# Optimization experiments

Hardware: AMD Instinct MI355X
Metric: run time of the kernel (lower is better)

## Reference

```python
import jax, jax.numpy as jnp
import numpy as np

R_BLOCKS = 8  # r: number of diagonal blocks

def _rotate(Wp, R):
    # Wp: [out, in], R: [r, b, b] with in = r*b.
    # Equivalent to Wp @ block_diag(R[0],...,R[r-1]) without materializing [in,in].
    o = Wp.shape[0]
    r, b, _ = R.shape
    Wb = Wp.reshape(o, r, b)
    return jnp.einsum('ori,rij->orj', Wb, R).reshape(o, r * b)

def setup_inputs() -> dict:
    key = jax.random.key(0)
    ks = jax.random.split(key, 6)
    in_f, out_f, r = 1024, 1024, R_BLOCKS
    blk = in_f // r
    return {
        'attn': jax.random.normal(ks[0], (3 * out_f, in_f), jnp.float32) * 0.02,
        'bias': jax.random.normal(ks[1], (3 * out_f,), jnp.float32) * 0.02,
        'x': jax.random.normal(ks[2], (4, 2048, in_f), jnp.float32),
        'q_R': jax.random.normal(ks[3], (r, blk, blk), jnp.float32) * 0.02,
        'k_R': jax.random.normal(ks[4], (r, blk, blk), jnp.float32) * 0.02,
        'v_R': jax.random.normal(ks[5], (r, blk, blk), jnp.float32) * 0.02,
    }

def reference(attn, bias, x, q_R, k_R, v_R):
    # attn.data in torch detaches the frozen pretrained weight
    W = jax.lax.stop_gradient(attn)
    Wq, Wk, Wv = jnp.split(W, 3, axis=0)
    filt = jnp.concatenate([_rotate(Wq, q_R), _rotate(Wk, k_R), _rotate(Wv, v_R)], axis=0)
    # F.linear: x @ filt.T + bias -> [B, S, 3*out]
    return jnp.einsum('bsi,oi->bso', x, filt) + bias
```

## Files before the change

kernel.cpp:

```cpp
#include <hip/hip_runtime.h>
#include <hip/hip_bf16.h>
#include <stdint.h>

typedef __attribute__((ext_vector_type(8))) short short8;
typedef __attribute__((ext_vector_type(4))) float floatx4;
typedef __attribute__((ext_vector_type(16))) float floatx16;

#define M_TOT 8192
#define N_TOT 3072
#define K_TOT 1024
#define BM 128
#define BN 128
#define BK 64

__device__ inline unsigned short f2bf(float f) {
    union { float f; unsigned int ui; } v; v.f = f;
    unsigned int x = v.ui;
    unsigned int r = (x + 0x7fffu + ((x >> 16) & 1u)) >> 16;
    return (unsigned short)r;
}

__device__ inline void gl2lds16(const void* g, void* l) {
    __builtin_amdgcn_global_load_lds(
        (__attribute__((address_space(1))) void*)g,
        (__attribute__((address_space(3))) void*)l,
        16, 0, 0);
}

__global__ __launch_bounds__(256) void cvt_f32_bf16_kernel(
    const float* __restrict__ in, unsigned short* __restrict__ out, int n8)
{
    int i = blockIdx.x * 256 + threadIdx.x;
    if (i >= n8) return;
    const float4* p = (const float4*)in + (size_t)i * 2;
    float4 a = p[0], b = p[1];
    short8 s;
    s[0] = (short)f2bf(a.x); s[1] = (short)f2bf(a.y);
    s[2] = (short)f2bf(a.z); s[3] = (short)f2bf(a.w);
    s[4] = (short)f2bf(b.x); s[5] = (short)f2bf(b.y);
    s[6] = (short)f2bf(b.z); s[7] = (short)f2bf(b.w);
    *(short8*)(out + (size_t)i * 8) = s;
}

__global__ __launch_bounds__(256) void rotate_w_kernel(
    const float* __restrict__ W,
    const float* __restrict__ qR,
    const float* __restrict__ kR,
    const float* __restrict__ vR,
    unsigned short* __restrict__ Fout)
{
    __shared__ float Rs[128 * 128];
    __shared__ float Ws[64 * 132];

    const int tid = threadIdx.x;
    const int o0 = blockIdx.x * 64;
    const int r = blockIdx.y;

    const float* R = (o0 < 1024) ? qR : (o0 < 2048) ? kR : vR;
    R += (size_t)r * 128 * 128;

#pragma unroll
    for (int i = 0; i < 16; ++i) {
        int idx = (i * 256 + tid) * 4;
        *(float4*)(Rs + idx) = *(const float4*)(R + idx);
    }
#pragma unroll
    for (int i = 0; i < 8; ++i) {
        int idx = (i * 256 + tid) * 4;
        int row = idx >> 7;
        int col = idx & 127;
        *(float4*)(Ws + row * 132 + col) =
            *(const float4*)(W + (size_t)(o0 + row) * K_TOT + r * 128 + col);
    }
    __syncthreads();

    const int jg = (tid & 15) * 8;
    const int ob = tid >> 4;

    float acc[4][8];
#pragma unroll
    for (int a = 0; a < 4; ++a)
#pragma unroll
        for (int b = 0; b < 8; ++b) acc[a][b] = 0.f;

    for (int i = 0; i < 128; ++i) {
        float4 r0 = *(const float4*)(Rs + i * 128 + jg);
        float4 r1 = *(const float4*)(Rs + i * 128 + jg + 4);
        float rv[8] = {r0.x, r0.y, r0.z, r0.w, r1.x, r1.y, r1.z, r1.w};
#pragma unroll
        for (int oo = 0; oo < 4; ++oo) {
            float wv = Ws[(ob + oo * 16) * 132 + i];
#pragma unroll
            for (int t = 0; t < 8; ++t) acc[oo][t] += wv * rv[t];
        }
    }

#pragma unroll
    for (int oo = 0; oo < 4; ++oo) {
        int o = o0 + ob + oo * 16;
        short8 s;
#pragma unroll
        for (int t = 0; t < 8; ++t) s[t] = (short)f2bf(acc[oo][t]);
        *(short8*)(Fout + (size_t)o * K_TOT + r * 128 + jg) = s;
    }
}

__global__ void gemm_bt_kernel(
    const unsigned short* __restrict__ X,
    const unsigned short* __restrict__ F,
    const float* __restrict__ bias,
    float* __restrict__ out)
{
    __shared__ __align__(16) unsigned char smem[2 * BM * BK * sizeof(unsigned short)];
    unsigned short* As = (unsigned short*)smem;
    unsigned short* Bs = As + BM * BK;
    float* Cs = (float*)smem;

    const int tid = threadIdx.x;
    const int wave = tid >> 6;
    const int lane = tid & 63;
    const int m0 = blockIdx.x * BM;
    const int n0 = blockIdx.y * BN;

    const int wm = wave >> 1;
    const int wn = wave & 1;
    const int l31 = lane & 31;
    const int khalf = lane >> 5;

    const int srow_lane = lane >> 3;

    floatx16 acc[2][2];
#pragma unroll
    for (int a = 0; a < 2; ++a)
#pragma unroll
        for (int b = 0; b < 2; ++b)
#pragma unroll
            for (int t = 0; t < 16; ++t) acc[a][b][t] = 0.f;

    const int fr_read = (l31 & 7) ^ (((l31 >> 3) & 3) << 1);

    for (int k0 = 0; k0 < K_TOT; k0 += BK) {
#pragma unroll
        for (int p = 0; p < 4; ++p) {
            const int rr = (wave * 4 + p) * 8 + srow_lane;
            const int scg = (lane & 7) ^ srow_lane ^ ((((wave * 4 + p) & 3)) << 1);
            const int scol = scg * 8;
            gl2lds16(X + (size_t)(m0 + rr) * K_TOT + k0 + scol,
                     As + (wave * 4 + p) * 512 + lane * 8);
            gl2lds16(F + (size_t)(n0 + rr) * K_TOT + k0 + scol,
                     Bs + (wave * 4 + p) * 512 + lane * 8);
        }
        __syncthreads();

#pragma unroll
        for (int ks = 0; ks < 4; ++ks) {
            const int fcg = ((ks * 2 + khalf) ^ fr_read) * 8;
            short8 a[2], b[2];
#pragma unroll
            for (int mi = 0; mi < 2; ++mi)
                a[mi] = *(const short8*)(As + (wm * 64 + mi * 32 + l31) * BK + fcg);
#pragma unroll
            for (int ni = 0; ni < 2; ++ni)
                b[ni] = *(const short8*)(Bs + (wn * 64 + ni * 32 + l31) * BK + fcg);
#pragma unroll
            for (int mi = 0; mi < 2; ++mi)
#pragma unroll
                for (int ni = 0; ni < 2; ++ni)
                    acc[mi][ni] = __builtin_amdgcn_mfma_f32_32x32x16_bf16(
                        a[mi], b[ni], acc[mi][ni], 0, 0, 0);
        }
        __syncthreads();
    }

    float bv[2];
#pragma unroll
    for (int ni = 0; ni < 2; ++ni)
        bv[ni] = bias[n0 + wn * 64 + ni * 32 + l31];

#pragma unroll
    for (int h = 0; h < 2; ++h) {
        if (wm == h) {
#pragma unroll
            for (int mi = 0; mi < 2; ++mi)
#pragma unroll
                for (int ni = 0; ni < 2; ++ni) {
                    const int col = wn * 64 + ni * 32 + l31;
#pragma unroll
                    for (int reg = 0; reg < 16; ++reg) {
                        const int row = mi * 32 + (reg & 3) + 8 * (reg >> 2) +
                                        4 * khalf;
                        Cs[row * 128 + col] = acc[mi][ni][reg] + bv[ni];
                    }
                }
        }
        __syncthreads();
#pragma unroll
        for (int t = 0; t < 8; ++t) {
            const int idx = t * 256 + tid;
            const int row = idx >> 5;
            const int c4 = (idx & 31) * 4;
            float4 v = *(const float4*)(Cs + row * 128 + c4);
            *(float4*)(out + (size_t)(m0 + h * 64 + row) * N_TOT + n0 + c4) = v;
        }
        __syncthreads();
    }
}

extern "C" void kernel_launch(void* const* d_in, const int* in_sizes, int n_in,
                              void* d_out, int out_size, void* d_ws, size_t ws_size,
                              hipStream_t stream) {
    const float* attn = (const float*)d_in[0];
    const float* bias = (const float*)d_in[1];
    const float* x    = (const float*)d_in[2];
    const float* qR   = (const float*)d_in[3];
    const float* kR   = (const float*)d_in[4];
    const float* vR   = (const float*)d_in[5];

    float* out = (float*)d_out;

    unsigned short* xb   = (unsigned short*)d_ws;
    unsigned short* filt = xb + (size_t)M_TOT * K_TOT;

    const int n8 = (M_TOT * K_TOT) / 8;
    cvt_f32_bf16_kernel<<<n8 / 256, 256, 0, stream>>>(x, xb, n8);
    rotate_w_kernel<<<dim3(48, 8), 256, 0, stream>>>(attn, qR, kR, vR, filt);
    gemm_bt_kernel<<<dim3(M_TOT / BM, N_TOT / BN), 256, 0, stream>>>(
        xb, filt, bias, out);
}
```

Baseline: 207.7 us.

## Replace GEMM with 256x256-tile, 8-wave, double-buffered pipelined MFMA kernel

Result: slower. 214.5 us (+3.3%).

```diff
diff --git a/kernel.cpp b/kernel.cpp
--- a/kernel.cpp
+++ b/kernel.cpp
@@ -4,14 +4,10 @@
 
 typedef __attribute__((ext_vector_type(8))) short short8;
 typedef __attribute__((ext_vector_type(4))) float floatx4;
-typedef __attribute__((ext_vector_type(16))) float floatx16;
 
 #define M_TOT 8192
 #define N_TOT 3072
 #define K_TOT 1024
-#define BM 128
-#define BN 128
-#define BK 64
 
 __device__ inline unsigned short f2bf(float f) {
     union { float f; unsigned int ui; } v; v.f = f;
@@ -105,105 +101,130 @@
     }
 }
 
-__global__ void gemm_bt_kernel(
+#define GKT 16
+
+__global__ __launch_bounds__(512, 2) void gemm256_kernel(
     const unsigned short* __restrict__ X,
     const unsigned short* __restrict__ F,
     const float* __restrict__ bias,
     float* __restrict__ out)
 {
-    __shared__ __align__(16) unsigned char smem[2 * BM * BK * sizeof(unsigned short)];
-    unsigned short* As = (unsigned short*)smem;
-    unsigned short* Bs = As + BM * BK;
-    float* Cs = (float*)smem;
+    extern __shared__ unsigned short sm[];
 
     const int tid = threadIdx.x;
-    const int wave = tid >> 6;
-    const int lane = tid & 63;
-    const int m0 = blockIdx.x * BM;
-    const int n0 = blockIdx.y * BN;
-
-    const int wm = wave >> 1;
-    const int wn = wave & 1;
-    const int l31 = lane & 31;
-    const int khalf = lane >> 5;
-
-    const int srow_lane = lane >> 3;
-
-    floatx16 acc[2][2];
-#pragma unroll
-    for (int a = 0; a < 2; ++a)
-#pragma unroll
-        for (int b = 0; b < 2; ++b)
-#pragma unroll
-            for (int t = 0; t < 16; ++t) acc[a][b][t] = 0.f;
-
-    const int fr_read = (l31 & 7) ^ (((l31 >> 3) & 3) << 1);
-
-    for (int k0 = 0; k0 < K_TOT; k0 += BK) {
-#pragma unroll
-        for (int p = 0; p < 4; ++p) {
-            const int rr = (wave * 4 + p) * 8 + srow_lane;
-            const int scg = (lane & 7) ^ srow_lane ^ ((((wave * 4 + p) & 3)) << 1);
-            const int scol = scg * 8;
-            gl2lds16(X + (size_t)(m0 + rr) * K_TOT + k0 + scol,
-                     As + (wave * 4 + p) * 512 + lane * 8);
-            gl2lds16(F + (size_t)(n0 + rr) * K_TOT + k0 + scol,
-                     Bs + (wave * 4 + p) * 512 + lane * 8);
+    const int wid = tid >> 6;
+    const int l   = tid & 63;
+    const int wm  = wid >> 2;
+    const int wn  = wid & 3;
+
+    const int bswz = (blockIdx.x & 7) * 48 + (blockIdx.x >> 3);
+    const int m0 = (bswz / 12) * 256;
+    const int n0 = (bswz % 12) * 256;
+
+    const int srow  = tid >> 3;
+    const int scb   = tid & 7;
+    const int sgcb  = scb ^ (srow & 7);
+    const int sswap = (tid >> 8) << 5;
+
+    const unsigned short* Xs = X + (size_t)(m0 + srow) * K_TOT + sgcb * 8;
+    const unsigned short* Fs = F + (size_t)(n0 + srow + sswap) * K_TOT + sgcb * 8;
+    unsigned short* smA = sm + srow * 64 + scb * 8;
+    unsigned short* smB = sm + 32768 + (srow + sswap) * 64 + scb * 8;
+
+#define STAGE_A(bo, rb, kc) gl2lds16(Xs + (size_t)(rb) * K_TOT + (kc), smA + (bo) + (rb) * 64)
+#define STAGE_B(bo, rb, kc) gl2lds16(Fs + (size_t)(rb) * K_TOT + (kc), smB + (bo) + (rb) * 64)
+#define STAGE_Ag0(bo, kc) { STAGE_A(bo, 0, kc);  STAGE_A(bo, 128, kc); }
+#define STAGE_Ag1(bo, kc) { STAGE_A(bo, 64, kc); STAGE_A(bo, 192, kc); }
+#define STAGE_Bg0(bo, kc) { STAGE_B(bo, 0, kc);  STAGE_B(bo, 128, kc); }
+#define STAGE_Bg1(bo, kc) { STAGE_B(bo, 32, kc); STAGE_B(bo, 160, kc); }
+#define BARRIER() asm volatile("s_barrier" ::: "memory")
+
+    const int l15 = l & 15;
+    const int s8a = (((l >> 4) + 0) ^ (l & 7)) * 8;
+    const int s8b = (((l >> 4) + 4) ^ (l & 7)) * 8;
+    const int paBase = (wm * 128 + l15) * 64;
+    const int pbBase = (wn * 64 + l15) * 64;
+
+    floatx4 acc[8][4];
+#pragma unroll
+    for (int i = 0; i < 8; ++i)
+#pragma unroll
+        for (int j = 0; j < 4; ++j)
+#pragma unroll
+            for (int t = 0; t < 4; ++t) acc[i][j][t] = 0.f;
+
+    short8 aF[4][2];
+    short8 bF[2][2][2];
+
+#define RD_A(QM, co) { _Pragma("unroll") for (int mf = 0; mf < 4; ++mf) { \
+        const unsigned short* p = sm + (co) + paBase + ((QM) * 4 + mf) * 1024; \
+        aF[mf][0] = *(const short8*)(p + s8a); \
+        aF[mf][1] = *(const short8*)(p + s8b); } }
+#define RD_B(QN, co) { _Pragma("unroll") for (int nf = 0; nf < 2; ++nf) { \
+        const unsigned short* p = sm + 32768 + (co) + pbBase + ((QN) * 2 + nf) * 1024; \
+        bF[QN][nf][0] = *(const short8*)(p + s8a); \
+        bF[QN][nf][1] = *(const short8*)(p + s8b); } }
+#define DO_MFMA(QM, QN) { __builtin_amdgcn_s_setprio(1); \
+        _Pragma("unroll") for (int mf = 0; mf < 4; ++mf) \
+        _Pragma("unroll") for (int nf = 0; nf < 2; ++nf) { \
+            acc[(QM)*4+mf][(QN)*2+nf] = __builtin_amdgcn_mfma_f32_16x16x32_bf16( \
+                aF[mf][0], bF[QN][nf][0], acc[(QM)*4+mf][(QN)*2+nf], 0, 0, 0); \
+            acc[(QM)*4+mf][(QN)*2+nf] = __builtin_amdgcn_mfma_f32_16x16x32_bf16( \
+                aF[mf][1], bF[QN][nf][1], acc[(QM)*4+mf][(QN)*2+nf], 0, 0, 0); } \
+        __builtin_amdgcn_s_setprio(0); }
+
+    STAGE_Ag0(0, 0); STAGE_Bg0(0, 0); STAGE_Bg1(0, 0); STAGE_Ag1(0, 0);
+    STAGE_Ag0(16384, 64); STAGE_Bg0(16384, 64);
+    asm volatile("s_waitcnt vmcnt(4)" ::: "memory");
+    BARRIER();
+
+    for (int kt = 0; kt < GKT; ++kt) {
+        const int co = (kt & 1) << 14;
+        const int no = co ^ 16384;
+        const int kc1 = (kt + 1) * 64;
+        const int kc2 = (kt + 2) * 64;
+
+        RD_A(0, co); RD_B(0, co);
+        if (kt + 1 < GKT) { STAGE_Bg1(no, kc1); }
+        BARRIER();
+        DO_MFMA(0, 0);
+        BARRIER();
+
+        RD_B(1, co);
+        if (kt + 1 < GKT) { STAGE_Ag1(no, kc1); }
+        BARRIER();
+        DO_MFMA(0, 1);
+        BARRIER();
+
+        RD_A(1, co);
+        if (kt + 2 < GKT) { STAGE_Ag0(co, kc2); }
+        BARRIER();
+        DO_MFMA(1, 0);
+        BARRIER();
+
+        if (kt + 2 < GKT) { STAGE_Bg0(co, kc2); }
+        if (kt < GKT - 2) { asm volatile("s_waitcnt vmcnt(4)" ::: "memory"); }
+        else              { asm volatile("s_waitcnt vmcnt(0)" ::: "memory"); }
+        BARRIER();
+        DO_MFMA(1, 1);
+        BARRIER();
+    }
+
+    float bv[4];
+#pragma unroll
+    for (int nf = 0; nf < 4; ++nf) bv[nf] = bias[n0 + wn * 64 + nf * 16 + l15];
+
+    const int mrow = m0 + wm * 128 + (l >> 4) * 4;
+    const int ncol = n0 + wn * 64 + l15;
+#pragma unroll
+    for (int mf = 0; mf < 8; ++mf)
+#pragma unroll
+        for (int nf = 0; nf < 4; ++nf) {
+            float* po = out + (size_t)(mrow + mf * 16) * N_TOT + ncol + nf * 16;
+#pragma unroll
+            for (int r = 0; r < 4; ++r)
+                po[(size_t)r * N_TOT] = acc[mf][nf][r] + bv[nf];
         }
-        __syncthreads();
-
-#pragma unroll
-        for (int ks = 0; ks < 4; ++ks) {
-            const int fcg = ((ks * 2 + khalf) ^ fr_read) * 8;
-            short8 a[2], b[2];
-#pragma unroll
-            for (int mi = 0; mi < 2; ++mi)
-                a[mi] = *(const short8*)(As + (wm * 64 + mi * 32 + l31) * BK + fcg);
-#pragma unroll
-            for (int ni = 0; ni < 2; ++ni)
-                b[ni] = *(const short8*)(Bs + (wn * 64 + ni * 32 + l31) * BK + fcg);
-#pragma unroll
-            for (int mi = 0; mi < 2; ++mi)
-#pragma unroll
-                for (int ni = 0; ni < 2; ++ni)
-                    acc[mi][ni] = __builtin_amdgcn_mfma_f32_32x32x16_bf16(
-                        a[mi], b[ni], acc[mi][ni], 0, 0, 0);
-        }
-        __syncthreads();
-    }
-
-    float bv[2];
-#pragma unroll
-    for (int ni = 0; ni < 2; ++ni)
-        bv[ni] = bias[n0 + wn * 64 + ni * 32 + l31];
-
-#pragma unroll
-    for (int h = 0; h < 2; ++h) {
-        if (wm == h) {
-#pragma unroll
-            for (int mi = 0; mi < 2; ++mi)
-#pragma unroll
-                for (int ni = 0; ni < 2; ++ni) {
-                    const int col = wn * 64 + ni * 32 + l31;
-#pragma unroll
-                    for (int reg = 0; reg < 16; ++reg) {
-                        const int row = mi * 32 + (reg & 3) + 8 * (reg >> 2) +
-                                        4 * khalf;
-                        Cs[row * 128 + col] = acc[mi][ni][reg] + bv[ni];
-                    }
-                }
-        }
-        __syncthreads();
-#pragma unroll
-        for (int t = 0; t < 8; ++t) {
-            const int idx = t * 256 + tid;
-            const int row = idx >> 5;
-            const int c4 = (idx & 31) * 4;
-            float4 v = *(const float4*)(Cs + row * 128 + c4);
-            *(float4*)(out + (size_t)(m0 + h * 64 + row) * N_TOT + n0 + c4) = v;
-        }
-        __syncthreads();
-    }
 }
 
 extern "C" void kernel_launch(void* const* d_in, const int* in_sizes, int n_in,
@@ -221,9 +242,15 @@
     unsigned short* xb   = (unsigned short*)d_ws;
     unsigned short* filt = xb + (size_t)M_TOT * K_TOT;
 
+    static bool attr_set = false;
+    if (!attr_set) {
+        hipFuncSetAttribute((const void*)gemm256_kernel,
+                            hipFuncAttributeMaxDynamicSharedMemorySize, 131072);
+        attr_set = true;
+    }
+
     const int n8 = (M_TOT * K_TOT) / 8;
     cvt_f32_bf16_kernel<<<n8 / 256, 256, 0, stream>>>(x, xb, n8);
     rotate_w_kernel<<<dim3(48, 8), 256, 0, stream>>>(attn, qR, kR, vR, filt);
-    gemm_bt_kernel<<<dim3(M_TOT / BM, N_TOT / BN), 256, 0, stream>>>(
-        xb, filt, bias, out);
-}
+    gemm256_kernel<<<dim3(384), dim3(512), 131072, stream>>>(xb, filt, bias, out);
+}
```
